# Performance work log

Measured on AMD Instinct MI355X. Metric: run time of the kernel, lower is better.

Reference implementation:

```python
import jax, jax.numpy as jnp
import numpy as np
from jax import lax

P = 4
PSIZE = P * P
ITERS = 3
EPS = 1e-8
LAMBDA = 1e-3  # inverse-temperature used by the EM routing sigmoid (yl-1993 style)
LN2PI_HALF = 0.5 * float(np.log(2.0 * np.pi))


def extract_patches(x, K, stride, pad):
    """x: (b,h,w,c) -> (b,oh,ow,K*K,c) sliding-window patches."""
    if pad:
        x = jnp.pad(x, ((0, 0), (pad, pad), (pad, pad), (0, 0)))
    b, h, w, c = x.shape
    oh = (h - K) // stride + 1
    ow = (w - K) // stride + 1
    slices = []
    for ki in range(K):
        for kj in range(K):
            slices.append(x[:, ki:ki + stride * (oh - 1) + 1:stride,
                             kj:kj + stride * (ow - 1) + 1:stride, :])
    return jnp.stack(slices, axis=3)  # (b,oh,ow,K*K,c)


def em_routing(v, a_in, beta_u, beta_a, iters=ITERS):
    """EM routing (Hinton et al. 2018).
    v: (n, Bin, Cout, PSIZE) votes, a_in: (n, Bin, 1) input activations.
    Returns mu: (n, Cout, PSIZE), a_out: (n, Cout).
    """
    n, Bin, Cout, psize = v.shape
    r = jnp.full((n, Bin, Cout), 1.0 / Cout, dtype=v.dtype)
    mu = None
    a_out = None
    for it in range(iters):
        # ---- M step ----
        r_w = r * a_in                                    # (n,Bin,Cout)
        r_sum = r_w.sum(axis=1, keepdims=True)            # (n,1,Cout)
        coeff = (r_w / (r_sum + EPS))[..., None]          # (n,Bin,Cout,1)
        mu = jnp.sum(coeff * v, axis=1, keepdims=True)    # (n,1,Cout,psize)
        sigma_sq = jnp.sum(coeff * (v - mu) ** 2, axis=1, keepdims=True) + EPS
        cost_h = (beta_u[None, None, :, None] + 0.5 * jnp.log(sigma_sq)) * r_sum[..., None]
        a_out = jax.nn.sigmoid(LAMBDA * (beta_a[None, None, :] - cost_h.sum(axis=3)))  # (n,1,Cout)
        # ---- E step ----
        if it < iters - 1:
            ln_p = -(v - mu) ** 2 / (2.0 * sigma_sq) - 0.5 * jnp.log(sigma_sq) - LN2PI_HALF
            ln_ap = ln_p.sum(axis=3) + jnp.log(EPS + a_out)  # (n,Bin,Cout)
            r = jax.nn.softmax(ln_ap, axis=2)
    return mu[:, 0], a_out[:, 0]


def depthwise_caps(pose, a, W, bu, ba, K, stride):
    """DepthWiseConvCaps: each capsule type routes its own KxK spatial patch to one
    output capsule of the same type. W: (K*K, B, P, P)."""
    b = pose.shape[0]
    Bc = a.shape[-1]
    pad = K // 2
    pp = extract_patches(pose, K, stride, pad)  # (b,oh,ow,KK,B*PSIZE)
    ap = extract_patches(a, K, stride, pad)     # (b,oh,ow,KK,B)
    oh, ow = pp.shape[1], pp.shape[2]
    pm = pp.reshape(b, oh, ow, K * K, Bc, P, P)
    v = jnp.einsum('bhwkcij,kcjl->bhwkcil', pm, W)            # (b,oh,ow,KK,B,P,P)
    v = v.transpose(0, 1, 2, 4, 3, 5, 6).reshape(b * oh * ow * Bc, K * K, 1, PSIZE)
    a_in = ap.transpose(0, 1, 2, 4, 3).reshape(b * oh * ow * Bc, K * K, 1)
    mu, a_out = em_routing(v, a_in, bu, ba)
    return mu.reshape(b, oh, ow, Bc * PSIZE), a_out.reshape(b, oh, ow, Bc)


def conv_caps_1x1(pose, a, W, bu, ba):
    """ConvCaps with K=1, stride=1: per-position routing Bin -> Cout. W: (Bin,Cout,P,P)."""
    b, h, w, _ = pose.shape
    Bc, Cc = W.shape[0], W.shape[1]
    pm = pose.reshape(b * h * w, Bc, P, P)
    v = jnp.einsum('nbij,bcjl->nbcil', pm, W).reshape(b * h * w, Bc, Cc, PSIZE)
    a_in = a.reshape(b * h * w, Bc)[..., None]
    mu, a_out = em_routing(v, a_in, bu, ba)
    return mu.reshape(b, h, w, Cc * PSIZE), a_out.reshape(b, h, w, Cc)


def class_caps(pose, a, W, bu, ba):
    """Class ConvCaps: w_shared across positions + coordinate addition. W: (D,E,P,P)."""
    b, h, w, _ = pose.shape
    D, E = W.shape[0], W.shape[1]
    pm = pose.reshape(b, h, w, D, P, P)
    v = jnp.einsum('bhwdij,dejl->bhwdeil', pm, W).reshape(b, h, w, D, E, PSIZE)
    # coordinate addition on the first two vote components
    coord = jnp.zeros((h, w, PSIZE), v.dtype)
    coord = coord.at[:, :, 0].add(jnp.arange(h, dtype=v.dtype)[:, None] / h)
    coord = coord.at[:, :, 1].add(jnp.arange(w, dtype=v.dtype)[None, :] / w)
    v = v + coord[None, :, :, None, None, :]
    v = v.reshape(b, h * w * D, E, PSIZE)
    a_in = a.reshape(b, h * w * D, 1)
    mu, a_out = em_routing(v, a_in, bu, ba)
    return mu, a_out  # (b,E,PSIZE), (b,E)


def _forward(x, conv1_w, conv1_b, prim_pose_w, prim_pose_b, prim_a_w, prim_a_b,
             dw1_w, dw1_bu, dw1_ba, cc1_w, cc1_bu, cc1_ba,
             dw2_w, dw2_bu, dw2_ba, cc2_w, cc2_bu, cc2_ba,
             cls_w, cls_bu, cls_ba):
    # conv stem: k5 s2 valid
    y = lax.conv_general_dilated(x, conv1_w, (2, 2), 'VALID',
                                 dimension_numbers=('NHWC', 'HWIO', 'NHWC'))
    y = jax.nn.relu(y + conv1_b)
    # primary caps: 1x1 convs for pose and activation
    pose = jnp.einsum('bhwc,cd->bhwd', y, prim_pose_w) + prim_pose_b   # (b,h,w,B*PSIZE)
    a = jax.nn.sigmoid(jnp.einsum('bhwc,cd->bhwd', y, prim_a_w) + prim_a_b)  # (b,h,w,B)
    pose, a = depthwise_caps(pose, a, dw1_w, dw1_bu, dw1_ba, K=7, stride=2)
    pose, a = conv_caps_1x1(pose, a, cc1_w, cc1_bu, cc1_ba)
    pose, a = depthwise_caps(pose, a, dw2_w, dw2_bu, dw2_ba, K=5, stride=2)
    pose, a = conv_caps_1x1(pose, a, cc2_w, cc2_bu, cc2_ba)
    pose_cls, a_cls = class_caps(pose, a, cls_w, cls_bu, cls_ba)
    return a_cls  # (b, E)


def setup_inputs() -> dict:
    key = jax.random.key(0)
    ks = jax.random.split(key, 10)
    f32 = jnp.float32
    d = {}
    d['x'] = jax.random.normal(ks[0], (32, 64, 64, 1), f32)
    d['conv1_w'] = jax.random.normal(ks[1], (5, 5, 1, 64), f32) * 0.1
    d['conv1_b'] = jnp.zeros((64,), f32)
    d['prim_pose_w'] = jax.random.normal(ks[2], (64, 128), f32) * 0.1
    d['prim_pose_b'] = jnp.zeros((128,), f32)
    d['prim_a_w'] = jax.random.normal(ks[3], (64, 8), f32) * 0.1
    d['prim_a_b'] = jnp.zeros((8,), f32)
    d['dw1_w'] = jax.random.normal(ks[4], (49, 8, 4, 4), f32) * 0.25
    d['dw1_bu'] = jnp.zeros((1,), f32)
    d['dw1_ba'] = jnp.zeros((1,), f32)
    d['cc1_w'] = jax.random.normal(ks[5], (8, 16, 4, 4), f32) * 0.25
    d['cc1_bu'] = jnp.zeros((16,), f32)
    d['cc1_ba'] = jnp.zeros((16,), f32)
    d['dw2_w'] = jax.random.normal(ks[6], (25, 16, 4, 4), f32) * 0.25
    d['dw2_bu'] = jnp.zeros((1,), f32)
    d['dw2_ba'] = jnp.zeros((1,), f32)
    d['cc2_w'] = jax.random.normal(ks[7], (16, 16, 4, 4), f32) * 0.25
    d['cc2_bu'] = jnp.zeros((16,), f32)
    d['cc2_ba'] = jnp.zeros((16,), f32)
    d['cls_w'] = jax.random.normal(ks[8], (16, 10, 4, 4), f32) * 0.25
    d['cls_bu'] = jnp.zeros((10,), f32)
    d['cls_ba'] = jnp.zeros((10,), f32)
    return d


def reference(x, conv1_w, conv1_b, prim_pose_w, prim_pose_b, prim_a_w, prim_a_b,
              dw1_w, dw1_bu, dw1_ba, cc1_w, cc1_bu, cc1_ba,
              dw2_w, dw2_bu, dw2_ba, cc2_w, cc2_bu, cc2_ba,
              cls_w, cls_bu, cls_ba):
    return _forward(x, conv1_w, conv1_b, prim_pose_w, prim_pose_b, prim_a_w, prim_a_b,
                    dw1_w, dw1_bu, dw1_ba, cc1_w, cc1_bu, cc1_ba,
                    dw2_w, dw2_bu, dw2_ba, cc2_w, cc2_bu, cc2_ba,
                    cls_w, cls_bu, cls_ba)
```

## Files before the change

kernel.cpp:

```cpp
#include <hip/hip_runtime.h>
#include <hip/hip_bf16.h>

#define EPS 1e-8f
#define LAMBDA 1e-3f
#define LN2PI_HALF 0.9189385332046727f

__device__ __forceinline__ float sigmoidf(float x) { return 1.f / (1.f + __expf(-x)); }

__global__ __launch_bounds__(256) void stem_primary_kernel(
    const float* __restrict__ x, const float* __restrict__ w,
    const float* __restrict__ bias,
    const float* __restrict__ wp, const float* __restrict__ bp,
    const float* __restrict__ wa, const float* __restrict__ ba,
    float* __restrict__ pose, float* __restrict__ a) {
  __shared__ float wp_s[64][128];
  __shared__ float wc_s[25][64];
  __shared__ float wa_s[64][8];
  __shared__ float bias_s[64];
  __shared__ float bp_s[128];
  __shared__ float ba_s[8];
  __shared__ float xs[5][23];
  __shared__ float ys[10][64];

  int t = threadIdx.x;
  int jt = blockIdx.x % 3;
  int oi = (blockIdx.x / 3) % 30;
  int b  = blockIdx.x / 90;
  int oj0 = jt * 10;

  for (int q = t; q < 8192; q += 256) ((float*)wp_s)[q] = wp[q];
  for (int q = t; q < 1600; q += 256) ((float*)wc_s)[q] = w[q];
  for (int q = t; q < 512;  q += 256) ((float*)wa_s)[q] = wa[q];
  if (t < 64) bias_s[t] = bias[t];
  if (t < 128) bp_s[t] = bp[t];
  if (t < 8) ba_s[t] = ba[t];
  for (int q = t; q < 115; q += 256) {
    int ki = q / 23, kj = q % 23;
    xs[ki][kj] = x[(b * 64 + 2 * oi + ki) * 64 + 2 * oj0 + kj];
  }
  __syncthreads();

#pragma unroll
  for (int rep = 0; rep < 3; ++rep) {
    int q = rep * 256 + t;
    if (q < 640) {
      int pos = q >> 6, ch = q & 63;
      float s = bias_s[ch];
#pragma unroll
      for (int ki = 0; ki < 5; ++ki)
#pragma unroll
        for (int kj = 0; kj < 5; ++kj)
          s += xs[ki][2 * pos + kj] * wc_s[ki * 5 + kj][ch];
      ys[pos][ch] = fmaxf(s, 0.f);
    }
  }
  __syncthreads();

  int w_ = t >> 7, d = t & 127;
  float acc[5];
#pragma unroll
  for (int j = 0; j < 5; ++j) acc[j] = bp_s[d];
  for (int c = 0; c < 64; ++c) {
    float wv = wp_s[c][d];
#pragma unroll
    for (int j = 0; j < 5; ++j) acc[j] += ys[w_ + 2 * j][c] * wv;
  }
  size_t rowbase = (size_t)(b * 30 + oi) * 30 + oj0;
#pragma unroll
  for (int j = 0; j < 5; ++j)
    pose[(rowbase + w_ + 2 * j) * 128 + d] = acc[j];

  if (t < 80) {
    int pos = t >> 3, jj = t & 7;
    float s = ba_s[jj];
#pragma unroll 8
    for (int c = 0; c < 64; ++c) s += ys[pos][c] * wa_s[c][jj];
    a[(rowbase + pos) * 8 + jj] = sigmoidf(s);
  }
}

template <int K, int BC, int HIN, int WIN, int HOUT, int WOUT, int OIG, int NG>
__global__ __launch_bounds__(256) void dw_caps_kernel(
    const float* __restrict__ pose_in, const float* __restrict__ a_in,
    const float* __restrict__ Wt,
    const float* __restrict__ bu_p, const float* __restrict__ ba_p,
    float* __restrict__ pose_out, float* __restrict__ a_out) {
  constexpr int PAD = K / 2;
  constexpr int RA = (2 * (OIG - 1) + K < HIN) ? (2 * (OIG - 1) + K) : HIN;
  __shared__ float tp[RA * WIN * 20];
  __shared__ float ta[RA * WIN];
  __shared__ float wt[K * K * 16];

  int t = threadIdx.x;
  int g = (NG > 1) ? (blockIdx.x % NG) : 0;
  int c = (blockIdx.x / NG) % BC;
  int b = blockIdx.x / (NG * BC);
  int oi_lo = g * OIG;
  int rlo = max(0, 2 * oi_lo - PAD);
  int rhi = min(HIN, 2 * (oi_lo + OIG - 1) - PAD + K);
  int nrows = rhi - rlo;

  for (int q = t; q < K * K * 16; q += 256) {
    int tap = q >> 4, lj = q & 15, l = lj >> 2, j = lj & 3;
    wt[tap * 16 + lj] = Wt[((size_t)tap * BC + c) * 16 + j * 4 + l];
  }
  for (int q = t; q < nrows * WIN; q += 256) {
    int row = q / WIN, col = q % WIN;
    ta[q] = a_in[((size_t)((b * HIN + rlo + row) * WIN + col)) * BC + c];
  }
  for (int q = t; q < nrows * WIN * 4; q += 256) {
    int quad = q & 3, pc = q >> 2;
    int row = pc / WIN, col = pc % WIN;
    const float4 src = *(const float4*)(pose_in +
        (((size_t)((b * HIN + rlo + row) * WIN + col)) * BC + c) * 16 + quad * 4);
    *(float4*)(tp + (row * WIN + col) * 20 + quad * 4) = src;
  }
  __syncthreads();

  for (int s = t; s < OIG * WOUT * 16; s += 256) {
    int p = s & 15, pr = s >> 4;
    int oj = pr % WOUT;
    int oi = oi_lo + pr / WOUT;
    int ip = p >> 2, l = p & 3;
    int ih0 = 2 * oi - PAD, iw0 = 2 * oj - PAD;
    float rsum = 0.f, acc = 0.f, acc2 = 0.f;
#pragma unroll
    for (int ki = 0; ki < K; ++ki) {
      int ih = ih0 + ki;
      if (ih < 0 || ih >= HIN) continue;
      int rbase = (ih - rlo) * WIN;
#pragma unroll
      for (int kj = 0; kj < K; ++kj) {
        int iw = iw0 + kj;
        if (iw < 0 || iw >= WIN) continue;
        float ak = ta[rbase + iw];
        const float4 pm = *(const float4*)(tp + (rbase + iw) * 20 + ip * 4);
        const float4 wr = *(const float4*)(wt + (ki * K + kj) * 16 + l * 4);
        float v = pm.x * wr.x + pm.y * wr.y + pm.z * wr.z + pm.w * wr.w;
        rsum += ak;
        float av = ak * v;
        acc += av;
        acc2 += av * v;
      }
    }
    float inv = 1.f / (rsum + EPS);
    float mu = acc * inv;
    float S = rsum * inv;
    float sg = acc2 * inv - mu * mu * (2.f - S);
    sg = fmaxf(sg, 0.f) + EPS;
    float hl = 0.5f * __logf(sg);
    float ls = hl;
    ls += __shfl_xor(ls, 1, 64);
    ls += __shfl_xor(ls, 2, 64);
    ls += __shfl_xor(ls, 4, 64);
    ls += __shfl_xor(ls, 8, 64);

    size_t obase = ((size_t)(b * HOUT + oi) * WOUT + oj) * BC + c;
    pose_out[obase * 16 + p] = mu;
    if (p == 0) {
      float cost = rsum * (16.f * bu_p[0] + ls);
      a_out[obase] = sigmoidf(LAMBDA * (ba_p[0] - cost));
    }
  }
}

template <int BIN>
__global__ __launch_bounds__(256) void cc_em_kernel(
    const float* __restrict__ pose_in, const float* __restrict__ a_arr,
    const float* __restrict__ Wt,
    const float* __restrict__ bu_p, const float* __restrict__ ba_p,
    float* __restrict__ pose_out, float* __restrict__ a_out) {
  constexpr int COUT = 16;
  __shared__ float wt_s[BIN * COUT * 20];
  int t = threadIdx.x;
  for (int idx = t; idx < BIN * COUT * 16; idx += 256) {
    int lk = idx & 15, l = lk >> 2, k = lk & 3;
    int bc = idx >> 4;
    wt_s[bc * 20 + l * 4 + k] = Wt[bc * 16 + k * 4 + l];
  }
  __syncthreads();

  int wave = t >> 6, lane = t & 63;
  int n = blockIdx.x * 4 + wave;
  int c = lane >> 2;
  int q = lane & 3;

  float ain[BIN], rw[BIN];
  float4 pmq[BIN];
#pragma unroll
  for (int b = 0; b < BIN; ++b) {
    ain[b] = a_arr[(size_t)n * BIN + b];
    rw[b] = (1.f / 16.f) * ain[b];
    pmq[b] = *(const float4*)(pose_in + (size_t)n * BIN * 16 + b * 16 + q * 4);
  }
  float bu = bu_p[c], ba = ba_p[c];

  float v[BIN][4];
#pragma unroll
  for (int b = 0; b < BIN; ++b) {
    const float* wr = wt_s + (b * 16 + c) * 20;
#pragma unroll
    for (int l = 0; l < 4; ++l) {
      const float4 w4 = *(const float4*)(wr + l * 4);
      v[b][l] = pmq[b].x * w4.x + pmq[b].y * w4.y + pmq[b].z * w4.z + pmq[b].w * w4.w;
    }
  }

  float mu[4], inv2[4], lsum = 0.f, ao = 0.f;
  for (int it = 0; it < 3; ++it) {
    float sA = 0.f, sV[4] = {0, 0, 0, 0}, sV2[4] = {0, 0, 0, 0};
#pragma unroll
    for (int b = 0; b < BIN; ++b) {
      sA += rw[b];
#pragma unroll
      for (int l = 0; l < 4; ++l) {
        float rv = rw[b] * v[b][l];
        sV[l] += rv;
        sV2[l] += rv * v[b][l];
      }
    }
    float inv = 1.f / (sA + EPS);
    float S = sA * inv;
    lsum = 0.f;
#pragma unroll
    for (int l = 0; l < 4; ++l) {
      mu[l] = sV[l] * inv;
      float sg = sV2[l] * inv - mu[l] * mu[l] * (2.f - S) + EPS;
      sg = fmaxf(sg, EPS);
      inv2[l] = 0.5f / sg;
      lsum += 0.5f * __logf(sg);
    }
    lsum += __shfl_xor(lsum, 1, 64);
    lsum += __shfl_xor(lsum, 2, 64);
    float cost = sA * (16.f * bu + lsum);
    ao = sigmoidf(LAMBDA * (ba - cost));

    if (it < 2) {
      float term[BIN];
#pragma unroll
      for (int b = 0; b < BIN; ++b) {
        float s = 0.f;
#pragma unroll
        for (int l = 0; l < 4; ++l) {
          float d = v[b][l] - mu[l];
          s += d * d * inv2[l];
        }
        term[b] = s;
      }
#pragma unroll
      for (int b = 0; b < BIN; ++b) {
        term[b] += __shfl_xor(term[b], 1, 64);
        term[b] += __shfl_xor(term[b], 2, 64);
      }
      float basec = __logf(EPS + ao) - lsum - 16.f * LN2PI_HALF;
      float lnap[BIN], Z[BIN];
#pragma unroll
      for (int b = 0; b < BIN; ++b) lnap[b] = basec - term[b];
      float mx[BIN];
#pragma unroll
      for (int b = 0; b < BIN; ++b) mx[b] = lnap[b];
#pragma unroll
      for (int m = 4; m < 64; m <<= 1)
#pragma unroll
        for (int b = 0; b < BIN; ++b) mx[b] = fmaxf(mx[b], __shfl_xor(mx[b], m, 64));
#pragma unroll
      for (int b = 0; b < BIN; ++b) { lnap[b] = __expf(lnap[b] - mx[b]); Z[b] = lnap[b]; }
#pragma unroll
      for (int m = 4; m < 64; m <<= 1)
#pragma unroll
        for (int b = 0; b < BIN; ++b) Z[b] += __shfl_xor(Z[b], m, 64);
#pragma unroll
      for (int b = 0; b < BIN; ++b) rw[b] = lnap[b] / Z[b] * ain[b];
    }
  }
  float4 om = make_float4(mu[0], mu[1], mu[2], mu[3]);
  *(float4*)(pose_out + (size_t)n * 256 + c * 16 + q * 4) = om;
  if (q == 0) a_out[(size_t)n * COUT + c] = ao;
}

__global__ __launch_bounds__(256) void cls_m_kernel(
    const float* __restrict__ pose5, const float* __restrict__ a5,
    const float* __restrict__ X, const float* __restrict__ W,
    const float* __restrict__ bu_p, const float* __restrict__ ba_p,
    float* __restrict__ mu_g, float* __restrict__ inv2_g,
    float* __restrict__ base_g, float* __restrict__ out,
    int first, int last) {
  int blk = blockIdx.x;
  int c = blk % 10, b = blk / 10;
  int t = threadIdx.x;
  int lane = t & 63, wv = t >> 6;
  const float* pg = pose5 + (size_t)b * 16384;
  __shared__ float w_s[16][16];
  {
    int d = t & 15, jj = t >> 4;
    w_s[jj][d] = W[(d * 10 + c) * 16 + jj];
  }
  __syncthreads();
  const int d = t & 15;
  float wf[16];
#pragma unroll
  for (int jj = 0; jj < 16; ++jj) wf[jj] = w_s[jj][d];

  float sA = 0.f, sV[16], sV2[16];
#pragma unroll
  for (int p = 0; p < 16; ++p) { sV[p] = 0.f; sV2[p] = 0.f; }
#pragma unroll
  for (int rep = 0; rep < 4; ++rep) {
    int bi = rep * 256 + t;
    int pos = bi >> 4;
    float rw = first ? 0.1f * a5[(size_t)b * 1024 + bi]
                     : X[(size_t)blk * 1024 + bi];
    float ci = (float)(pos >> 3) * 0.125f;
    float cj = (float)(pos & 7) * 0.125f;
    const float* pp = pg + pos * 256 + d * 16;
    float pmr[16];
#pragma unroll
    for (int q = 0; q < 16; ++q) pmr[q] = pp[q];
    sA += rw;
#pragma unroll
    for (int p = 0; p < 16; ++p) {
      int ip = p >> 2, l = p & 3;
      float v = pmr[ip * 4 + 0] * wf[0 * 4 + l] + pmr[ip * 4 + 1] * wf[1 * 4 + l]
              + pmr[ip * 4 + 2] * wf[2 * 4 + l] + pmr[ip * 4 + 3] * wf[3 * 4 + l];
      if (p == 0) v += ci;
      else if (p == 1) v += cj;
      float rv = rw * v;
      sV[p] += rv;
      sV2[p] += rv * v;
    }
  }
#pragma unroll
  for (int off = 1; off < 64; off <<= 1) {
    sA += __shfl_xor(sA, off, 64);
#pragma unroll
    for (int p = 0; p < 16; ++p) {
      sV[p]  += __shfl_xor(sV[p],  off, 64);
      sV2[p] += __shfl_xor(sV2[p], off, 64);
    }
  }
  __shared__ float red[4][36];
  if (lane == 0) {
    red[wv][0] = sA;
#pragma unroll
    for (int p = 0; p < 16; ++p) { red[wv][1 + p] = sV[p]; red[wv][17 + p] = sV2[p]; }
  }
  __syncthreads();
  if (t < 16) {
    int p = t;
    float sAf  = red[0][0] + red[1][0] + red[2][0] + red[3][0];
    float sVf  = red[0][1+p] + red[1][1+p] + red[2][1+p] + red[3][1+p];
    float sV2f = red[0][17+p] + red[1][17+p] + red[2][17+p] + red[3][17+p];
    float inv = 1.f / (sAf + EPS);
    float S = sAf * inv;
    float mu = sVf * inv;
    float sg = sV2f * inv - mu * mu * (2.f - S) + EPS;
    sg = fmaxf(sg, EPS);
    mu_g[blk * 16 + p] = mu;
    inv2_g[blk * 16 + p] = 0.5f / sg;
    float hl = 0.5f * __logf(sg);
    float lsum = hl;
    lsum += __shfl_xor(lsum, 1, 64);
    lsum += __shfl_xor(lsum, 2, 64);
    lsum += __shfl_xor(lsum, 4, 64);
    lsum += __shfl_xor(lsum, 8, 64);
    if (p == 0) {
      float cost = sAf * (16.f * bu_p[c] + lsum);
      float ao = sigmoidf(LAMBDA * (ba_p[c] - cost));
      base_g[blk] = __logf(EPS + ao) - lsum - 16.f * LN2PI_HALF;
      if (last) out[blk] = ao;
    }
  }
}

__global__ __launch_bounds__(512) void cls_e_kernel(
    const float* __restrict__ pose5, const float* __restrict__ a5,
    const float* __restrict__ W,
    const float* __restrict__ mu_g, const float* __restrict__ inv2_g,
    const float* __restrict__ base_g, float* __restrict__ X) {
  int b = blockIdx.x >> 1;
  int t = threadIdx.x;
  int bi = ((blockIdx.x & 1) << 9) + t;
  const float* pg = pose5 + (size_t)b * 16384;
  __shared__ float w2[10][16][16];
  __shared__ float mu_s[160];
  __shared__ float inv2_s[160];
  __shared__ float base_s[10];
  for (int q = t; q < 2560; q += 512) {
    int dd = q & 15, jj = (q >> 4) & 15, c = q >> 8;
    w2[c][jj][dd] = W[(dd * 10 + c) * 16 + jj];
  }
  if (t < 160) { mu_s[t] = mu_g[b * 160 + t]; inv2_s[t] = inv2_g[b * 160 + t]; }
  if (t >= 160 && t < 170) base_s[t - 160] = base_g[b * 10 + (t - 160)];
  __syncthreads();

  int pos = bi >> 4, d2 = bi & 15;
  float ci = (float)(pos >> 3) * 0.125f;
  float cj = (float)(pos & 7) * 0.125f;
  const float* pp = pg + pos * 256 + d2 * 16;
  float pmr[16];
#pragma unroll
  for (int q = 0; q < 16; ++q) pmr[q] = pp[q];
  float lnap[10];
#pragma unroll
  for (int c = 0; c < 10; ++c) {
    float wf[16];
#pragma unroll
    for (int jj = 0; jj < 16; ++jj) wf[jj] = w2[c][jj][d2];
    float s = base_s[c];
#pragma unroll
    for (int p = 0; p < 16; ++p) {
      int ip = p >> 2, l = p & 3;
      float v = pmr[ip * 4 + 0] * wf[0 * 4 + l] + pmr[ip * 4 + 1] * wf[1 * 4 + l]
              + pmr[ip * 4 + 2] * wf[2 * 4 + l] + pmr[ip * 4 + 3] * wf[3 * 4 + l];
      if (p == 0) v += ci;
      else if (p == 1) v += cj;
      float dd = v - mu_s[c * 16 + p];
      s -= dd * dd * inv2_s[c * 16 + p];
    }
    lnap[c] = s;
  }
  float m = -1e30f;
#pragma unroll
  for (int c = 0; c < 10; ++c) m = fmaxf(m, lnap[c]);
  float Z = 0.f;
  float ex[10];
#pragma unroll
  for (int c = 0; c < 10; ++c) { ex[c] = __expf(lnap[c] - m); Z += ex[c]; }
  float invZ = a5[(size_t)b * 1024 + bi] / Z;
#pragma unroll
  for (int c = 0; c < 10; ++c) X[((size_t)(b * 10 + c)) * 1024 + bi] = ex[c] * invZ;
}

extern "C" void kernel_launch(void* const* d_in, const int* in_sizes, int n_in,
                              void* d_out, int out_size, void* d_ws, size_t ws_size,
                              hipStream_t stream) {
  const float* x       = (const float*)d_in[0];
  const float* conv1_w = (const float*)d_in[1];
  const float* conv1_b = (const float*)d_in[2];
  const float* pp_w    = (const float*)d_in[3];
  const float* pp_b    = (const float*)d_in[4];
  const float* pa_w    = (const float*)d_in[5];
  const float* pa_b    = (const float*)d_in[6];
  const float* dw1_w   = (const float*)d_in[7];
  const float* dw1_bu  = (const float*)d_in[8];
  const float* dw1_ba  = (const float*)d_in[9];
  const float* cc1_w   = (const float*)d_in[10];
  const float* cc1_bu  = (const float*)d_in[11];
  const float* cc1_ba  = (const float*)d_in[12];
  const float* dw2_w   = (const float*)d_in[13];
  const float* dw2_bu  = (const float*)d_in[14];
  const float* dw2_ba  = (const float*)d_in[15];
  const float* cc2_w   = (const float*)d_in[16];
  const float* cc2_bu  = (const float*)d_in[17];
  const float* cc2_ba  = (const float*)d_in[18];
  const float* cls_w   = (const float*)d_in[19];
  const float* cls_bu  = (const float*)d_in[20];
  const float* cls_ba  = (const float*)d_in[21];
  float* out = (float*)d_out;

  float* ws = (float*)d_ws;
  float* pose1 = ws;
  float* a1    = ws + 3686400;
  float* pose2 = ws + 3916800;
  float* a2    = ws + 4838400;
  float* pose3 = ws;
  float* a3    = ws + 1843200;
  float* pose4 = ws + 1958400;
  float* a4    = ws + 2482688;
  float* pose5 = ws + 2515456;
  float* a5    = ws + 3039744;
  float* Xbuf  = ws + 3072512;
  float* mu_g  = ws + 3400192;
  float* inv2_g= ws + 3405312;
  float* base_g= ws + 3410432;

  stem_primary_kernel<<<2880, 256, 0, stream>>>(x, conv1_w, conv1_b,
                                                pp_w, pp_b, pa_w, pa_b, pose1, a1);
  dw_caps_kernel<7, 8, 30, 30, 15, 15, 5, 3><<<768, 256, 0, stream>>>(
      pose1, a1, dw1_w, dw1_bu, dw1_ba, pose2, a2);
  cc_em_kernel<8><<<1800, 256, 0, stream>>>(pose2, a2, cc1_w, cc1_bu, cc1_ba, pose3, a3);
  dw_caps_kernel<5, 16, 15, 15, 8, 8, 8, 1><<<512, 256, 0, stream>>>(
      pose3, a3, dw2_w, dw2_bu, dw2_ba, pose4, a4);
  cc_em_kernel<16><<<512, 256, 0, stream>>>(pose4, a4, cc2_w, cc2_bu, cc2_ba, pose5, a5);
  cls_m_kernel<<<320, 256, 0, stream>>>(pose5, a5, Xbuf, cls_w, cls_bu, cls_ba,
                                        mu_g, inv2_g, base_g, out, 1, 0);
  cls_e_kernel<<<64, 512, 0, stream>>>(pose5, a5, cls_w, mu_g, inv2_g, base_g, Xbuf);
  cls_m_kernel<<<320, 256, 0, stream>>>(pose5, a5, Xbuf, cls_w, cls_bu, cls_ba,
                                        mu_g, inv2_g, base_g, out, 0, 0);
  cls_e_kernel<<<64, 512, 0, stream>>>(pose5, a5, cls_w, mu_g, inv2_g, base_g, Xbuf);
  cls_m_kernel<<<320, 256, 0, stream>>>(pose5, a5, Xbuf, cls_w, cls_bu, cls_ba,
                                        mu_g, inv2_g, base_g, out, 0, 1);
}
```

Before: 266.6 us.

## Process full output rows in stem block and compute 4 pose cols per dw thread

The stem/primary kernel now gives each block a whole 30-wide output row instead of a 10-wide third. The 32KB weight tile is loaded into shared memory a third as often and each thread accumulates 15 outputs with float4 shared reads. The depthwise caps kernel makes each thread compute a full 4-wide row of the vote matrix, reusing the pose and activation loads across four columns and writing float4 outputs. In exchange the stem grid drops to 960 blocks, each thread holds more registers, and the dw kernel has fewer active threads.

Result: slower. 284.0 us (+6.5%).

```diff
diff --git a/kernel.cpp b/kernel.cpp
--- a/kernel.cpp
+++ b/kernel.cpp
@@ -19,14 +19,12 @@
   __shared__ float bias_s[64];
   __shared__ float bp_s[128];
   __shared__ float ba_s[8];
-  __shared__ float xs[5][23];
-  __shared__ float ys[10][64];
+  __shared__ float xs[5][63];
+  __shared__ float ys_u[2][15][68];
 
   int t = threadIdx.x;
-  int jt = blockIdx.x % 3;
-  int oi = (blockIdx.x / 3) % 30;
-  int b  = blockIdx.x / 90;
-  int oj0 = jt * 10;
+  int oi = blockIdx.x % 30;
+  int b  = blockIdx.x / 30;
 
   for (int q = t; q < 8192; q += 256) ((float*)wp_s)[q] = wp[q];
   for (int q = t; q < 1600; q += 256) ((float*)wc_s)[q] = w[q];
@@ -34,48 +32,51 @@
   if (t < 64) bias_s[t] = bias[t];
   if (t < 128) bp_s[t] = bp[t];
   if (t < 8) ba_s[t] = ba[t];
-  for (int q = t; q < 115; q += 256) {
-    int ki = q / 23, kj = q % 23;
-    xs[ki][kj] = x[(b * 64 + 2 * oi + ki) * 64 + 2 * oj0 + kj];
-  }
-  __syncthreads();
-
-#pragma unroll
-  for (int rep = 0; rep < 3; ++rep) {
-    int q = rep * 256 + t;
-    if (q < 640) {
-      int pos = q >> 6, ch = q & 63;
-      float s = bias_s[ch];
-#pragma unroll
-      for (int ki = 0; ki < 5; ++ki)
-#pragma unroll
-        for (int kj = 0; kj < 5; ++kj)
-          s += xs[ki][2 * pos + kj] * wc_s[ki * 5 + kj][ch];
-      ys[pos][ch] = fmaxf(s, 0.f);
-    }
+  for (int q = t; q < 315; q += 256) {
+    int ki = q / 63, col = q % 63;
+    xs[ki][col] = x[(b * 64 + 2 * oi + ki) * 64 + col];
+  }
+  __syncthreads();
+
+  for (int q = t; q < 1920; q += 256) {
+    int pos = q >> 6, ch = q & 63;
+    float s = bias_s[ch];
+#pragma unroll
+    for (int ki = 0; ki < 5; ++ki)
+#pragma unroll
+      for (int kj = 0; kj < 5; ++kj)
+        s += xs[ki][2 * pos + kj] * wc_s[ki * 5 + kj][ch];
+    ys_u[pos & 1][pos >> 1][ch] = fmaxf(s, 0.f);
   }
   __syncthreads();
 
   int w_ = t >> 7, d = t & 127;
-  float acc[5];
-#pragma unroll
-  for (int j = 0; j < 5; ++j) acc[j] = bp_s[d];
-  for (int c = 0; c < 64; ++c) {
-    float wv = wp_s[c][d];
-#pragma unroll
-    for (int j = 0; j < 5; ++j) acc[j] += ys[w_ + 2 * j][c] * wv;
-  }
-  size_t rowbase = (size_t)(b * 30 + oi) * 30 + oj0;
-#pragma unroll
-  for (int j = 0; j < 5; ++j)
-    pose[(rowbase + w_ + 2 * j) * 128 + d] = acc[j];
-
-  if (t < 80) {
+  float acc[15];
+#pragma unroll
+  for (int j = 0; j < 15; ++j) acc[j] = bp_s[d];
+#pragma unroll 4
+  for (int c4 = 0; c4 < 64; c4 += 4) {
+    float w0 = wp_s[c4 + 0][d];
+    float w1 = wp_s[c4 + 1][d];
+    float w2 = wp_s[c4 + 2][d];
+    float w3 = wp_s[c4 + 3][d];
+#pragma unroll
+    for (int j = 0; j < 15; ++j) {
+      const float4 yv = *(const float4*)&ys_u[w_][j][c4];
+      acc[j] += yv.x * w0 + yv.y * w1 + yv.z * w2 + yv.w * w3;
+    }
+  }
+  size_t rowb = (size_t)(b * 30 + oi) * 30;
+#pragma unroll
+  for (int j = 0; j < 15; ++j)
+    pose[(rowb + w_ + 2 * j) * 128 + d] = acc[j];
+
+  if (t < 240) {
     int pos = t >> 3, jj = t & 7;
     float s = ba_s[jj];
 #pragma unroll 8
-    for (int c = 0; c < 64; ++c) s += ys[pos][c] * wa_s[c][jj];
-    a[(rowbase + pos) * 8 + jj] = sigmoidf(s);
+    for (int c = 0; c < 64; ++c) s += ys_u[pos & 1][pos >> 1][c] * wa_s[c][jj];
+    a[(rowb + pos) * 8 + jj] = sigmoidf(s);
   }
 }
 
@@ -100,10 +101,8 @@
   int rhi = min(HIN, 2 * (oi_lo + OIG - 1) - PAD + K);
   int nrows = rhi - rlo;
 
-  for (int q = t; q < K * K * 16; q += 256) {
-    int tap = q >> 4, lj = q & 15, l = lj >> 2, j = lj & 3;
-    wt[tap * 16 + lj] = Wt[((size_t)tap * BC + c) * 16 + j * 4 + l];
-  }
+  for (int q = t; q < K * K * 16; q += 256)
+    wt[q] = Wt[((size_t)(q >> 4) * BC + c) * 16 + (q & 15)];
   for (int q = t; q < nrows * WIN; q += 256) {
     int row = q / WIN, col = q % WIN;
     ta[q] = a_in[((size_t)((b * HIN + rlo + row) * WIN + col)) * BC + c];
@@ -117,13 +116,13 @@
   }
   __syncthreads();
 
-  for (int s = t; s < OIG * WOUT * 16; s += 256) {
-    int p = s & 15, pr = s >> 4;
+  for (int s = t; s < OIG * WOUT * 4; s += 256) {
+    int ip = s & 3, pr = s >> 2;
     int oj = pr % WOUT;
     int oi = oi_lo + pr / WOUT;
-    int ip = p >> 2, l = p & 3;
     int ih0 = 2 * oi - PAD, iw0 = 2 * oj - PAD;
-    float rsum = 0.f, acc = 0.f, acc2 = 0.f;
+    float rsum = 0.f;
+    float4 acc = make_float4(0, 0, 0, 0), acc2 = make_float4(0, 0, 0, 0);
 #pragma unroll
     for (int ki = 0; ki < K; ++ki) {
       int ih = ih0 + ki;
@@ -135,29 +134,38 @@
         if (iw < 0 || iw >= WIN) continue;
         float ak = ta[rbase + iw];
         const float4 pm = *(const float4*)(tp + (rbase + iw) * 20 + ip * 4);
-        const float4 wr = *(const float4*)(wt + (ki * K + kj) * 16 + l * 4);
-        float v = pm.x * wr.x + pm.y * wr.y + pm.z * wr.z + pm.w * wr.w;
+        const float* wb = wt + (ki * K + kj) * 16;
+        const float4 w0 = *(const float4*)(wb + 0);
+        const float4 w1 = *(const float4*)(wb + 4);
+        const float4 w2 = *(const float4*)(wb + 8);
+        const float4 w3 = *(const float4*)(wb + 12);
+        float4 v;
+        v.x = pm.x * w0.x + pm.y * w1.x + pm.z * w2.x + pm.w * w3.x;
+        v.y = pm.x * w0.y + pm.y * w1.y + pm.z * w2.y + pm.w * w3.y;
+        v.z = pm.x * w0.z + pm.y * w1.z + pm.z * w2.z + pm.w * w3.z;
+        v.w = pm.x * w0.w + pm.y * w1.w + pm.z * w2.w + pm.w * w3.w;
         rsum += ak;
-        float av = ak * v;
-        acc += av;
-        acc2 += av * v;
+        acc.x += ak * v.x;  acc2.x += ak * v.x * v.x;
+        acc.y += ak * v.y;  acc2.y += ak * v.y * v.y;
+        acc.z += ak * v.z;  acc2.z += ak * v.z * v.z;
+        acc.w += ak * v.w;  acc2.w += ak * v.w * v.w;
       }
     }
     float inv = 1.f / (rsum + EPS);
-    float mu = acc * inv;
     float S = rsum * inv;
-    float sg = acc2 * inv - mu * mu * (2.f - S);
-    sg = fmaxf(sg, 0.f) + EPS;
-    float hl = 0.5f * __logf(sg);
-    float ls = hl;
+    float4 mu, sg;
+    mu.x = acc.x * inv; mu.y = acc.y * inv; mu.z = acc.z * inv; mu.w = acc.w * inv;
+    sg.x = fmaxf(acc2.x * inv - mu.x * mu.x * (2.f - S), 0.f) + EPS;
+    sg.y = fmaxf(acc2.y * inv - mu.y * mu.y * (2.f - S), 0.f) + EPS;
+    sg.z = fmaxf(acc2.z * inv - mu.z * mu.z * (2.f - S), 0.f) + EPS;
+    sg.w = fmaxf(acc2.w * inv - mu.w * mu.w * (2.f - S), 0.f) + EPS;
+    float ls = 0.5f * (__logf(sg.x) + __logf(sg.y) + __logf(sg.z) + __logf(sg.w));
     ls += __shfl_xor(ls, 1, 64);
     ls += __shfl_xor(ls, 2, 64);
-    ls += __shfl_xor(ls, 4, 64);
-    ls += __shfl_xor(ls, 8, 64);
 
     size_t obase = ((size_t)(b * HOUT + oi) * WOUT + oj) * BC + c;
-    pose_out[obase * 16 + p] = mu;
-    if (p == 0) {
+    *(float4*)(pose_out + obase * 16 + ip * 4) = mu;
+    if (ip == 0) {
       float cost = rsum * (16.f * bu_p[0] + ls);
       a_out[obase] = sigmoidf(LAMBDA * (ba_p[0] - cost));
     }
@@ -474,8 +482,8 @@
   float* inv2_g= ws + 3405312;
   float* base_g= ws + 3410432;
 
-  stem_primary_kernel<<<2880, 256, 0, stream>>>(x, conv1_w, conv1_b,
-                                                pp_w, pp_b, pa_w, pa_b, pose1, a1);
+  stem_primary_kernel<<<960, 256, 0, stream>>>(x, conv1_w, conv1_b,
+                                               pp_w, pp_b, pa_w, pa_b, pose1, a1);
   dw_caps_kernel<7, 8, 30, 30, 15, 15, 5, 3><<<768, 256, 0, stream>>>(
       pose1, a1, dw1_w, dw1_bu, dw1_ba, pose2, a2);
   cc_em_kernel<8><<<1800, 256, 0, stream>>>(pose2, a2, cc1_w, cc1_bu, cc1_ba, pose3, a3);
```
